# Kernel tuning notes

Hardware: AMD Instinct MI355X
Metric: run time of the kernel (lower is better)

Reference implementation:

```python
import jax, jax.numpy as jnp
import numpy as np

NUM_EXPERTS = 64
SPATIAL_DIM = 3
SHARPNESS = 10.0
B = 1048576


def setup_inputs() -> dict:
    key = jax.random.key(0)
    k1, k2 = jax.random.split(key)
    positions_3d = jax.random.normal(k1, (B, SPATIAL_DIM), dtype=jnp.float32)
    centers = jax.random.normal(k2, (NUM_EXPERTS, SPATIAL_DIM), dtype=jnp.float32)
    radii = jnp.ones((NUM_EXPERTS,), dtype=jnp.float32) * 0.5
    return {"positions_3d": positions_3d, "centers": centers, "radii": radii}


def reference(positions_3d, centers, radii):
    # radii are made safe (abs, clamped min=0.01) as in _maybe_rebuild_gas/forward
    safe_radii = jnp.maximum(jnp.abs(radii), 0.01)  # (E,)
    # distance from each query position to each expert sphere center: (B, E)
    diff = positions_3d[:, None, :] - centers[None, :, :]  # (B, E, 3)
    dist = jnp.sqrt(jnp.sum(diff * diff, axis=-1) + 1e-12)
    # smooth hit score: positive inside the sphere, sharpness-scaled
    logits = SHARPNESS * (safe_radii[None, :] - dist)  # (B, E)
    soft = jax.nn.softmax(logits, axis=-1)
    # STE: hard one-hot (BVH hit / nearest sphere) in forward, soft grads in backward
    expert_ids = jnp.argmax(soft, axis=-1)  # (B,)
    hard = jax.nn.one_hot(expert_ids, NUM_EXPERTS, dtype=soft.dtype)
    expert_probs = hard + soft - jax.lax.stop_gradient(soft)
    return expert_probs, expert_ids
```

## Files before the change

### kernel.cpp

```cpp
#include <hip/hip_runtime.h>
#include <math.h>

#define NE 64
#define SHARP 10.0f

typedef float vf4 __attribute__((ext_vector_type(4)));

__global__ __launch_bounds__(256) void optix_route_kernel(
    const float* __restrict__ pos,
    const float* __restrict__ centers,
    const float* __restrict__ radii,
    float* __restrict__ probs,
    float* __restrict__ ids,
    long long nB)
{
#pragma clang fp contract(off)
    __shared__ float4 scr[NE];
    __shared__ int s_uni;
    const int t = threadIdx.x;
    if (t < NE) {
        float cx = centers[3*t+0], cy = centers[3*t+1], cz = centers[3*t+2];
        float sr = fmaxf(fabsf(radii[t]), 0.01f);
        scr[t] = make_float4(cx, cy, cz, sr);
        float sr0 = __shfl(sr, 0, 64);
        int uni = __all(sr == sr0);
        if (t == 0) s_uni = uni;
    }
    __syncthreads();

    const int lane = t & 63;
    const int wave = t >> 6;
    const long long base = ((long long)blockIdx.x * 4 + wave) * 64;
    if (base >= nB) return;
    const long long p = base + lane;

    const float x = pos[3*p+0];
    const float y = pos[3*p+1];
    const float z = pos[3*p+2];

    float m  = INFINITY;
    float m2 = INFINITY;
    int   am = 0;
    #pragma unroll
    for (int j = 0; j < NE; ++j) {
        const float4 c = scr[j];
        const float dx = x - c.x, dy = y - c.y, dz = z - c.z;
        const float s2 = __builtin_fmaf(dx, dx, __builtin_fmaf(dy, dy, dz * dz));
        const bool lt = s2 < m;
        m2 = lt ? m : fminf(m2, s2);
        am = lt ? j : am;
        m  = lt ? s2 : m;
    }

    int a = am;
    const bool risky = (!s_uni) || ((m2 - m) <= (m + 1e-12f) * 0x1.0p-16f);
    if (risky) {
        float mm = -INFINITY;
        for (int j = 0; j < NE; ++j) {
            const float4 c = scr[j];
            const float dx = x - c.x, dy = y - c.y, dz = z - c.z;
            const float s2 = (dx*dx + dy*dy) + dz*dz;
            const float d  = sqrtf(s2 + 1e-12f);
            const float lg = SHARP * (c.w - d);
            mm = fmaxf(mm, lg);
        }
        int idx_top = NE, idx_near = NE;
        for (int j = 0; j < NE; ++j) {
            const float4 c = scr[j];
            const float dx = x - c.x, dy = y - c.y, dz = z - c.z;
            const float s2 = (dx*dx + dy*dy) + dz*dz;
            const float d  = sqrtf(s2 + 1e-12f);
            const float lg = SHARP * (c.w - d);
            const float dlt = lg - mm;
            if (dlt >= -0x1.0p-25f)      { if (idx_top  == NE) idx_top  = j; }
            else if (dlt >= -0x1.8p-24f) { if (idx_near == NE) idx_near = j; }
        }
        a = (idx_top < NE) ? idx_top : am;
        if (idx_near < a) {
            const float ONE_M = 0x1.fffffep-1f;
            float r8[8];
            for (int q = 0; q < 8; ++q) r8[q] = 0.0f;
            for (int j = 0; j < NE; ++j) {
                const float4 c = scr[j];
                const float dx = x - c.x, dy = y - c.y, dz = z - c.z;
                const float s2 = (dx*dx + dy*dy) + dz*dz;
                const float d  = sqrtf(s2 + 1e-12f);
                const float lg = SHARP * (c.w - d);
                const float dlt = lg - mm;
                float e;
                if (dlt >= -0x1.0p-25f)      e = 1.0f;
                else if (dlt >= -0x1.8p-24f) e = ONE_M;
                else                         e = expf(dlt);
                r8[j & 7] = r8[j & 7] + e;
            }
            const float Z = ((r8[0]+r8[1]) + (r8[2]+r8[3]))
                          + ((r8[4]+r8[5]) + (r8[6]+r8[7]));
            if ((1.0f / Z) == (ONE_M / Z)) a = idx_near;
        }
    }

    {
        float* rowbase = probs + (size_t)base * 64;
        const int sub = lane & 7;
        #pragma unroll
        for (int it = 0; it < 8; ++it) {
            const int row   = it * 8 + (lane >> 3);
            const int ar    = __shfl(a, row, 64);
            const int cbase = ((ar >> 5) << 5) + (sub << 2);
            vf4 v;
            v.x = (cbase + 0 == ar) ? 1.0f : 0.0f;
            v.y = (cbase + 1 == ar) ? 1.0f : 0.0f;
            v.z = (cbase + 2 == ar) ? 1.0f : 0.0f;
            v.w = (cbase + 3 == ar) ? 1.0f : 0.0f;
            __builtin_nontemporal_store(v, (vf4*)(rowbase + (size_t)row * 64 + cbase));
        }
    }
    __builtin_nontemporal_store((float)a, &ids[p]);
}

extern "C" void kernel_launch(void* const* d_in, const int* in_sizes, int n_in,
                              void* d_out, int out_size, void* d_ws, size_t ws_size,
                              hipStream_t stream) {
    const float* pos     = (const float*)d_in[0];
    const float* centers = (const float*)d_in[1];
    const float* radii   = (const float*)d_in[2];
    const long long B = (long long)in_sizes[0] / 3;

    float* probs = (float*)d_out;
    float* ids   = probs + (size_t)B * NE;

    const int blocks = (int)((B + 255) / 256);
    optix_route_kernel<<<blocks, 256, 0, stream>>>(pos, centers, radii,
                                                   probs, ids, B);
}
```

Measured before the change: 272.0 us.

## Defer rare near-tie rows to a separate fix-up kernel via atomic worklist

The main kernel no longer runs the exact softmax tie-break inline. When a row's top two squared distances are nearly tied, or the radii are not uniform, it appends the row index to a workspace list with an atomic counter. A small second kernel then recomputes those rows exactly and rewrites their one-hot output. The intent is to shrink the hot kernel's code, register use and divergence, and to raise occupancy with a launch-bounds hint and partial unrolling. In exchange it adds two extra launches, a zeroing kernel and the fix-up kernel. Risky rows beyond the workspace capacity would be left unfixed.

```diff
diff --git a/kernel.cpp b/kernel.cpp
--- a/kernel.cpp
+++ b/kernel.cpp
@@ -6,7 +6,160 @@
 
 typedef float vf4 __attribute__((ext_vector_type(4)));
 
-__global__ __launch_bounds__(256) void optix_route_kernel(
+
+__global__ void zero_counter(unsigned int* rl) {
+    rl[0] = 0u;
+}
+
+__global__ __launch_bounds__(256, 6) void route_fast(
+    const float* __restrict__ pos,
+    const float* __restrict__ centers,
+    const float* __restrict__ radii,
+    float* __restrict__ probs,
+    float* __restrict__ ids,
+    unsigned int* __restrict__ rl,
+    unsigned int cap,
+    long long nB)
+{
+#pragma clang fp contract(off)
+    __shared__ float4 scr[NE];
+    __shared__ int s_uni;
+    const int t = threadIdx.x;
+    if (t < NE) {
+        float cx = centers[3*t+0], cy = centers[3*t+1], cz = centers[3*t+2];
+        float sr = fmaxf(fabsf(radii[t]), 0.01f);
+        scr[t] = make_float4(cx, cy, cz, sr);
+        float sr0 = __shfl(sr, 0, 64);
+        int uni = __all(sr == sr0);
+        if (t == 0) s_uni = uni;
+    }
+    __syncthreads();
+
+    const int lane = t & 63;
+    const int wave = t >> 6;
+    const long long base = ((long long)blockIdx.x * 4 + wave) * 64;
+    if (base >= nB) return;
+    const long long p = base + lane;
+
+    const float x = pos[3*p+0];
+    const float y = pos[3*p+1];
+    const float z = pos[3*p+2];
+
+    float m  = INFINITY;
+    float m2 = INFINITY;
+    int   am = 0;
+    #pragma unroll 16
+    for (int j = 0; j < NE; ++j) {
+        const float4 c = scr[j];
+        const float dx = x - c.x, dy = y - c.y, dz = z - c.z;
+        const float s2 = __builtin_fmaf(dx, dx, __builtin_fmaf(dy, dy, dz * dz));
+        const bool lt = s2 < m;
+        m2 = lt ? m : fminf(m2, s2);
+        am = lt ? j : am;
+        m  = lt ? s2 : m;
+    }
+
+    const bool risky = (!s_uni) || ((m2 - m) <= (m + 1e-12f) * 0x1.0p-16f);
+    if (__builtin_expect(risky, 0)) {
+        const unsigned int slot = atomicAdd(rl, 1u);
+        if (slot < cap) rl[1 + slot] = (unsigned int)p;
+    }
+    const int a = am;
+
+    {
+        float* rowbase = probs + (size_t)base * 64;
+        const int sub = lane & 7;
+        #pragma unroll
+        for (int it = 0; it < 8; ++it) {
+            const int row   = it * 8 + (lane >> 3);
+            const int ar    = __shfl(a, row, 64);
+            const int cbase = ((ar >> 5) << 5) + (sub << 2);
+            vf4 v;
+            v.x = (cbase + 0 == ar) ? 1.0f : 0.0f;
+            v.y = (cbase + 1 == ar) ? 1.0f : 0.0f;
+            v.z = (cbase + 2 == ar) ? 1.0f : 0.0f;
+            v.w = (cbase + 3 == ar) ? 1.0f : 0.0f;
+            __builtin_nontemporal_store(v, (vf4*)(rowbase + (size_t)row * 64 + cbase));
+        }
+    }
+    __builtin_nontemporal_store((float)a, &ids[p]);
+}
+
+__global__ __launch_bounds__(256) void route_fix(
+    const float* __restrict__ pos,
+    const float* __restrict__ centers,
+    const float* __restrict__ radii,
+    float* __restrict__ probs,
+    float* __restrict__ ids,
+    const unsigned int* __restrict__ rl,
+    unsigned int cap)
+{
+#pragma clang fp contract(off)
+    const unsigned int n0 = rl[0];
+    const unsigned int n  = n0 < cap ? n0 : cap;
+    for (unsigned int i = blockIdx.x * blockDim.x + threadIdx.x; i < n;
+         i += gridDim.x * blockDim.x) {
+        const unsigned int row = rl[1 + i];
+        const float x = pos[3*(size_t)row+0];
+        const float y = pos[3*(size_t)row+1];
+        const float z = pos[3*(size_t)row+2];
+
+        float mm = -INFINITY;
+        for (int j = 0; j < NE; ++j) {
+            const float dx = x - centers[3*j+0];
+            const float dy = y - centers[3*j+1];
+            const float dz = z - centers[3*j+2];
+            const float s2 = (dx*dx + dy*dy) + dz*dz;
+            const float d  = sqrtf(s2 + 1e-12f);
+            const float sr = fmaxf(fabsf(radii[j]), 0.01f);
+            const float lg = SHARP * (sr - d);
+            mm = fmaxf(mm, lg);
+        }
+        int idx_top = NE, idx_near = NE;
+        for (int j = 0; j < NE; ++j) {
+            const float dx = x - centers[3*j+0];
+            const float dy = y - centers[3*j+1];
+            const float dz = z - centers[3*j+2];
+            const float s2 = (dx*dx + dy*dy) + dz*dz;
+            const float d  = sqrtf(s2 + 1e-12f);
+            const float sr = fmaxf(fabsf(radii[j]), 0.01f);
+            const float lg = SHARP * (sr - d);
+            const float dlt = lg - mm;
+            if (dlt >= -0x1.0p-25f)      { if (idx_top  == NE) idx_top  = j; }
+            else if (dlt >= -0x1.8p-24f) { if (idx_near == NE) idx_near = j; }
+        }
+        int a = idx_top;
+        if (idx_near < a) {
+            const float ONE_M = 0x1.fffffep-1f;
+            float r8[8];
+            for (int q = 0; q < 8; ++q) r8[q] = 0.0f;
+            for (int j = 0; j < NE; ++j) {
+                const float dx = x - centers[3*j+0];
+                const float dy = y - centers[3*j+1];
+                const float dz = z - centers[3*j+2];
+                const float s2 = (dx*dx + dy*dy) + dz*dz;
+                const float d  = sqrtf(s2 + 1e-12f);
+                const float sr = fmaxf(fabsf(radii[j]), 0.01f);
+                const float lg = SHARP * (sr - d);
+                const float dlt = lg - mm;
+                float e;
+                if (dlt >= -0x1.0p-25f)      e = 1.0f;
+                else if (dlt >= -0x1.8p-24f) e = ONE_M;
+                else                         e = expf(dlt);
+                r8[j & 7] = r8[j & 7] + e;
+            }
+            const float Z = ((r8[0]+r8[1]) + (r8[2]+r8[3]))
+                          + ((r8[4]+r8[5]) + (r8[6]+r8[7]));
+            if ((1.0f / Z) == (ONE_M / Z)) a = idx_near;
+        }
+
+        float* rowp = probs + (size_t)row * 64;
+        for (int j = 0; j < NE; ++j) rowp[j] = (j == a) ? 1.0f : 0.0f;
+        ids[row] = (float)a;
+    }
+}
+
+__global__ __launch_bounds__(256) void optix_route_fallback(
     const float* __restrict__ pos,
     const float* __restrict__ centers,
     const float* __restrict__ radii,
@@ -130,6 +283,20 @@
     float* ids   = probs + (size_t)B * NE;
 
     const int blocks = (int)((B + 255) / 256);
-    optix_route_kernel<<<blocks, 256, 0, stream>>>(pos, centers, radii,
-                                                   probs, ids, B);
-}
+
+    if (d_ws == nullptr || ws_size < 4096) {
+        optix_route_fallback<<<blocks, 256, 0, stream>>>(pos, centers, radii,
+                                                         probs, ids, B);
+        return;
+    }
+
+    unsigned int* rl = (unsigned int*)d_ws;
+    unsigned long long cap_ll = ws_size / 4 - 1;
+    if (cap_ll > (unsigned long long)B) cap_ll = (unsigned long long)B;
+    const unsigned int cap = (unsigned int)cap_ll;
+
+    zero_counter<<<1, 1, 0, stream>>>(rl);
+    route_fast<<<blocks, 256, 0, stream>>>(pos, centers, radii,
+                                           probs, ids, rl, cap, B);
+    route_fix<<<64, 256, 0, stream>>>(pos, centers, radii, probs, ids, rl, cap);
+}
```

Result: slower. 285.6 us (+5.0%).
